# Optimization experiments

Hardware: AMD Instinct MI355X
Metric: run time of the kernel (lower is better)

The kernel has to match this reference:

```python
import jax, jax.numpy as jnp
import numpy as np

B = 32768
NM = 3      # number of modalities (len(mk))
NE = 8      # number of experts
D_IN = 768
D_P = 128   # per-modality projection dim
D_X = D_P * NM  # 384, concatenated feature dim


def setup_inputs() -> dict:
    key = jax.random.key(0)
    ks = jax.random.split(key, 16)
    s = 0.02
    return {
        "feat_text": jax.random.normal(ks[0], (B, D_IN), jnp.float32),
        "feat_audio": jax.random.normal(ks[1], (B, D_IN), jnp.float32),
        "feat_video": jax.random.normal(ks[2], (B, D_IN), jnp.float32),
        "proj_w": jax.random.normal(ks[3], (NM, D_IN, D_P), jnp.float32) * s,
        "proj_b": jax.random.normal(ks[4], (NM, D_P), jnp.float32) * s,
        "exp_w1": jax.random.normal(ks[5], (NE, D_X, D_P), jnp.float32) * s,
        "exp_b1": jax.random.normal(ks[6], (NE, D_P), jnp.float32) * s,
        "exp_w2": jax.random.normal(ks[7], (NE, D_P, D_P), jnp.float32) * s,
        "exp_b2": jax.random.normal(ks[8], (NE, D_P), jnp.float32) * s,
        "gate_w": jax.random.normal(ks[9], (D_X, NE), jnp.float32) * s,
        "gate_b": jax.random.normal(ks[10], (NE,), jnp.float32) * s,
        "pre_w": jax.random.normal(ks[11], (D_P, 64), jnp.float32) * s,
        "pre_b": jax.random.normal(ks[12], (64,), jnp.float32) * s,
        "head_w": jax.random.normal(ks[13], (64, 2), jnp.float32) * s,
        "head_b": jax.random.normal(ks[14], (2,), jnp.float32) * s,
    }


def reference(feat_text, feat_audio, feat_video, proj_w, proj_b,
              exp_w1, exp_b1, exp_w2, exp_b2, gate_w, gate_b,
              pre_w, pre_b, head_w, head_b):
    feats = jnp.stack([feat_text, feat_audio, feat_video], axis=0)  # [M,B,768]
    # per-modality projections, then concat: [B, 128*M]
    proj = jnp.einsum('mbd,mdp->mbp', feats, proj_w) + proj_b[:, None, :]
    x = jnp.concatenate(jnp.split(proj, NM, axis=0), axis=-1)[0]  # [B, 384]
    # gate: softmax over 8 experts
    gw = jax.nn.softmax(x @ gate_w + gate_b, axis=-1)  # [B, 8]
    # all experts as batched GEMM: [E,B,128]
    h = jax.nn.relu(jnp.einsum('bx,exh->ebh', x, exp_w1) + exp_b1[:, None, :])
    eo = jnp.einsum('ebh,eho->ebo', h, exp_w2) + exp_b2[:, None, :]
    fused = jnp.einsum('be,ebh->bh', gw, eo)  # weighted sum over experts
    penult = jax.nn.relu(fused @ pre_w + pre_b)  # Dropout is identity in eval
    logits = penult @ head_w + head_b  # [B, 2]
    return logits
```

## Files before the change

kernel.cpp:

```cpp
#include <hip/hip_runtime.h>
#include <hip/hip_bf16.h>

#define B_ROWS 32768

typedef unsigned short u16;
typedef unsigned int u32;
typedef float f32x4 __attribute__((ext_vector_type(4)));
typedef __bf16 bf16x8 __attribute__((ext_vector_type(8)));

__device__ __forceinline__ u16 f2bf(float f){
    union { float f; u32 u; } v; v.f = f;
    return (u16)((v.u + 0x7FFFu + ((v.u >> 16) & 1u)) >> 16);
}
__device__ __forceinline__ float bf2f(u16 h){
    union { u32 u; float f; } v; v.u = ((u32)h) << 16; return v.f;
}
__device__ __forceinline__ u32 cvtpk(float lo, float hi){
    u32 r;
    asm("v_cvt_pk_bf16_f32 %0, %1, %2" : "=v"(r) : "v"(lo), "v"(hi));
    return r;
}
__device__ __forceinline__ void async_cp16(void* lds_dst, const void* g_src){
    __builtin_amdgcn_global_load_lds(
        (const __attribute__((address_space(1))) unsigned int*)g_src,
        (__attribute__((address_space(3))) unsigned int*)lds_dst, 16, 0, 0);
}

__global__ void cast_weights_kernel(const float* __restrict__ proj_w,
                                    const float* __restrict__ exp_w1,
                                    const float* __restrict__ exp_w2,
                                    const float* __restrict__ pre_w,
                                    const float* __restrict__ gate_w,
                                    u16* __restrict__ pimg, u16* __restrict__ w1img,
                                    u16* __restrict__ w2img, u16* __restrict__ prwT,
                                    u16* __restrict__ gwimg){
    int i = blockIdx.x * 256 + threadIdx.x;
    if (i < 294912){
        int m = i / 98304, r = i % 98304;
        int c = r / 4096, rr = r % 4096;
        int col = rr >> 5, kk = rr & 31;
        int kb = kk ^ (((col >> 1) & 3) << 3);
        pimg[i] = f2bf(proj_w[m*98304 + (c*32 + kb)*128 + col]);
    } else if (i < 688128){
        int j = i - 294912;
        int e = j / 49152, r = j % 49152;
        int ph = r / 4096, rr = r % 4096;
        int q = rr >> 10, col = (rr >> 3) & 127, el = rr & 7;
        w1img[j] = f2bf(exp_w1[e*49152 + (ph*32 + q*8 + el)*128 + col]);
    } else if (i < 819200){
        int j = i - 688128;
        int e = j / 16384, r = j % 16384;
        int c2 = r / 4096, rr = r % 4096;
        int q = rr >> 10, col = (rr >> 3) & 127, el = rr & 7;
        w2img[j] = f2bf(exp_w2[e*16384 + (c2*32 + q*8 + el)*128 + col]);
    } else if (i < 827392){
        int j = i - 819200;
        int o = j / 128, k = j % 128;
        prwT[j] = f2bf(pre_w[k*64 + o]);
    } else if (i < 833536){
        int j = i - 827392;
        int e = j / 384, k = j % 384;
        gwimg[j] = (e < 8) ? f2bf(gate_w[k*8 + e]) : (u16)0;
    }
}

#define XS_OFF   0
#define A_OFF    98304
#define B_OFF    147456
#define HS_OFF   98304
#define GWT_OFF  131072
#define B1_OFF   135168
#define B2_OFF   137216
#define WB_OFF   139264

__global__ __launch_bounds__(512, 1) void fused_kernel(
    const float* __restrict__ ft, const float* __restrict__ fa, const float* __restrict__ fv,
    const u16* __restrict__ pimg, const float* __restrict__ proj_b,
    const u16* __restrict__ w1img, const u16* __restrict__ w2img,
    const u16* __restrict__ prwT, const u16* __restrict__ gwimg,
    const float* __restrict__ gate_b, const float* __restrict__ exp_b1, const float* __restrict__ exp_b2,
    const float* __restrict__ pre_b, const float* __restrict__ head_w, const float* __restrict__ head_b,
    float* __restrict__ out)
{
    __shared__ __align__(16) char lds[163840];
    const int tid = threadIdx.x;
    const int lane = tid & 63, wid = tid >> 6;
    const int wr = wid >> 1, wc = wid & 1;
    const int lr = lane & 15, q = lane >> 4;
    const int blk = blockIdx.x;
    const int row0 = blk * 128;
    const char* w1b = (const char*)w1img;
    const char* w2b = (const char*)w2img;
    char* HsB = lds + HS_OFF;
    u16* b1L = (u16*)(lds + B1_OFF);
    u16* b2L = (u16*)(lds + B2_OFF);

    float pb0[4], pb1[4], pb2[4];
    #pragma unroll
    for (int ni = 0; ni < 4; ni++){
        int c = wc*64 + ni*16 + lr;
        pb0[ni] = proj_b[c];
        pb1[ni] = proj_b[128 + c];
        pb2[ni] = proj_b[256 + c];
    }
    asm volatile("s_waitcnt vmcnt(0)" ::: "memory");

    u32 aoffs[2];
    #pragma unroll
    for (int i = 0; i < 2; i++){
        int P = i*8192 + tid*16;
        int row = P >> 7, inner = P & 127;
        aoffs[i] = (u32)((row0 + row)*3072 + (inner ^ ((row & 7) << 4)));
    }

#define ASTAGE(c) do{                                                          \
        int mm_ = (c) / 24, kk_ = (c) % 24;                                    \
        const char* ab_ = (const char*)(mm_ == 0 ? ft : mm_ == 1 ? fa : fv);   \
        char* la_ = lds + A_OFF + ((c) % 3)*16384 + tid*16;                    \
        async_cp16(la_,        ab_ + aoffs[0] + kk_*128);                      \
        async_cp16(la_ + 8192, ab_ + aoffs[1] + kk_*128);                      \
    }while(0)

#define BSTAGE(c) do{                                                          \
        int mm_ = (c) / 24, kk_ = (c) % 24;                                    \
        async_cp16(lds + B_OFF + ((c) % 2)*8192 + tid*16,                      \
                   (const char*)pimg + mm_*196608 + kk_*8192 + tid*16);        \
    }while(0)

#define PCONSUME(c) do{                                                        \
        const char* Abuf = lds + A_OFF + ((c) % 3)*16384;                      \
        const char* Bbuf = lds + B_OFF + ((c) % 2)*8192;                       \
        bf16x8 af[2];                                                          \
        _Pragma("unroll")                                                      \
        for (int mi = 0; mi < 2; mi++){                                        \
            int row = wr*32 + mi*16 + lr;                                      \
            int aoff = row*128 + ((q*32) ^ ((row & 7) << 4));                  \
            f32x4 a0 = *(const f32x4*)(Abuf + aoff);                           \
            f32x4 a1 = *(const f32x4*)(Abuf + (aoff ^ 16));                    \
            union { u32 w[4]; bf16x8 v; } u;                                   \
            u.w[0] = cvtpk(a0.x, a0.y); u.w[1] = cvtpk(a0.z, a0.w);            \
            u.w[2] = cvtpk(a1.x, a1.y); u.w[3] = cvtpk(a1.z, a1.w);            \
            af[mi] = u.v;                                                      \
        }                                                                      \
        __builtin_amdgcn_s_setprio(1);                                         \
        _Pragma("unroll")                                                      \
        for (int ni = 0; ni < 4; ni++){                                        \
            int col = wc*64 + ni*16 + lr;                                      \
            int boff = col*64 + ((q*16) ^ (((col >> 1) & 3) << 4));            \
            bf16x8 bf = *(const bf16x8*)(Bbuf + boff);                         \
            acc[0][ni] = __builtin_amdgcn_mfma_f32_16x16x32_bf16(af[0], bf, acc[0][ni], 0, 0, 0); \
            acc[1][ni] = __builtin_amdgcn_mfma_f32_16x16x32_bf16(af[1], bf, acc[1][ni], 0, 0, 0); \
        }                                                                      \
        __builtin_amdgcn_s_setprio(0);                                         \
    }while(0)

#define PHASE_A_MOD(MC, PB) do{                                                \
        _Pragma("unroll 1")                                                    \
        for (int kt = 0; kt < 24; kt++){                                       \
            int t = MC*24 + kt;                                                \
            __builtin_amdgcn_sched_barrier(0);                                 \
            __builtin_amdgcn_s_barrier();                                      \
            if (t < 71) BSTAGE(t + 1);                                         \
            if (t < 70) ASTAGE(t + 2);                                         \
            if (t < 70)       asm volatile("s_waitcnt vmcnt(5)" ::: "memory"); \
            else if (t == 70) asm volatile("s_waitcnt vmcnt(3)" ::: "memory"); \
            else              asm volatile("s_waitcnt vmcnt(0)" ::: "memory"); \
            __builtin_amdgcn_s_barrier();                                      \
            __builtin_amdgcn_sched_barrier(0);                                 \
            PCONSUME(t);                                                       \
        }                                                                      \
        _Pragma("unroll")                                                      \
        for (int mi = 0; mi < 2; mi++)                                         \
            _Pragma("unroll")                                                  \
            for (int ni = 0; ni < 4; ni++){                                    \
                int lcol = wc*64 + ni*16 + lr;                                 \
                int colg = MC*128 + lcol;                                      \
                int ktI = colg >> 5, qI = (colg >> 3) & 3, el = colg & 7;      \
                _Pragma("unroll")                                              \
                for (int j = 0; j < 4; j++){                                   \
                    int row = wr*32 + mi*16 + q*4 + j;                         \
                    *(u16*)(lds + (row >> 6)*49152 + ktI*4096 + qI*1024        \
                            + (row & 63)*16 + el*2) = f2bf(acc[mi][ni][j] + PB[ni]); \
                    acc[mi][ni][j] = 0.f;                                      \
                }                                                              \
            }                                                                  \
    }while(0)

    f32x4 acc[2][4];
    #pragma unroll
    for (int i = 0; i < 2; i++)
        #pragma unroll
        for (int j = 0; j < 4; j++) acc[i][j] = {0.f, 0.f, 0.f, 0.f};

    BSTAGE(0); ASTAGE(0); ASTAGE(1);
    PHASE_A_MOD(0, pb0);
    PHASE_A_MOD(1, pb1);
    PHASE_A_MOD(2, pb2);
#undef ASTAGE
#undef BSTAGE
#undef PCONSUME
#undef PHASE_A_MOD

    asm volatile("s_waitcnt lgkmcnt(0)" ::: "memory");
    __builtin_amdgcn_sched_barrier(0);
    __builtin_amdgcn_s_barrier();

    bf16x8 xreg[12][2];
    {
        const char* xa0 = lds + (wr >> 1)*49152 + q*1024;
        #pragma unroll
        for (int ph = 0; ph < 12; ph++){
            xreg[ph][0] = *(const bf16x8*)(xa0 + ph*4096 + ((wr & 1)*32 + lr)*16);
            xreg[ph][1] = *(const bf16x8*)(xa0 + ph*4096 + ((wr & 1)*32 + 16 + lr)*16);
        }
    }

    {
        const char* src = w1b + tid*16;
        async_cp16(lds + WB_OFF + 0*8192 + tid*16, src);
        async_cp16(lds + WB_OFF + 1*8192 + tid*16, src + 8192);
        async_cp16(lds + WB_OFF + 2*8192 + tid*16, src + 16384);
    }
    for (int i = tid; i < 1024; i += 512){
        b1L[i] = f2bf(exp_b1[i]);
        b2L[i] = f2bf(exp_b2[i]);
    }
    {
        f32x4 ga = {0.f, 0.f, 0.f, 0.f};
        const char* xb = lds + (wid >> 2)*49152 + ((wid & 3)*16 + lr)*16 + q*1024;
        const u16* gwp = gwimg + lr*384 + q*8;
        #pragma unroll
        for (int kt = 0; kt < 12; kt++){
            bf16x8 af = *(const bf16x8*)(xb + kt*4096);
            bf16x8 gb = *(const bf16x8*)(gwp + kt*32);
            ga = __builtin_amdgcn_mfma_f32_16x16x32_bf16(af, gb, ga, 0, 0, 0);
        }
        float gbv = gate_b[lr & 7];
        float gw4[4];
        #pragma unroll
        for (int j = 0; j < 4; j++){
            float v = ga[j] + gbv;
            float mx = v;
            mx = fmaxf(mx, __shfl_xor(mx, 1));
            mx = fmaxf(mx, __shfl_xor(mx, 2));
            mx = fmaxf(mx, __shfl_xor(mx, 4));
            float s = __expf(v - mx);
            float t = s;
            t += __shfl_xor(t, 1);
            t += __shfl_xor(t, 2);
            t += __shfl_xor(t, 4);
            gw4[j] = s / t;
        }
        if (lr < 8){
            f32x4 wv = {gw4[0], gw4[1], gw4[2], gw4[3]};
            *(f32x4*)(lds + GWT_OFF + lr*512 + (wid*16 + q*4)*4) = wv;
        }
    }
    asm volatile("s_waitcnt vmcnt(0) lgkmcnt(0)" ::: "memory");
    __builtin_amdgcn_sched_barrier(0);
    __builtin_amdgcn_s_barrier();

#define WGROUP_STAGE(gg2) do{                                                  \
        int e2_ = (gg2) / 6, i2_ = (gg2) % 6;                                  \
        if (i2_ < 4){                                                          \
            const char* src_ = w1b + e2_*98304 + i2_*3*8192 + tid*16;          \
            async_cp16(lds + WB_OFF + 0*8192 + tid*16, src_);                  \
            async_cp16(lds + WB_OFF + 1*8192 + tid*16, src_ + 8192);           \
            async_cp16(lds + WB_OFF + 2*8192 + tid*16, src_ + 16384);          \
        } else {                                                               \
            const char* src_ = w2b + e2_*32768 + (i2_ - 4)*2*8192 + tid*16;    \
            async_cp16(lds + WB_OFF + 0*8192 + tid*16, src_);                  \
            async_cp16(lds + WB_OFF + 1*8192 + tid*16, src_ + 8192);           \
        }                                                                      \
    }while(0)

    f32x4 fus[2][4];
    #pragma unroll
    for (int i = 0; i < 2; i++)
        #pragma unroll
        for (int j = 0; j < 4; j++) fus[i][j] = {0.f, 0.f, 0.f, 0.f};

    #pragma unroll 1
    for (int e = 0; e < 8; e++){
        f32x4 ac1[2][4];
        #pragma unroll
        for (int i = 0; i < 2; i++)
            #pragma unroll
            for (int j = 0; j < 4; j++) ac1[i][j] = {0.f, 0.f, 0.f, 0.f};

        #pragma unroll
        for (int grp = 0; grp < 4; grp++){
            __builtin_amdgcn_s_setprio(1);
            #pragma unroll
            for (int c = 0; c < 3; c++){
                int ph = grp*3 + c;
                const char* wsl = lds + WB_OFF + c*8192 + q*2048;
                #pragma unroll
                for (int ni = 0; ni < 4; ni++){
                    bf16x8 bf = *(const bf16x8*)(wsl + (wc*64 + ni*16 + lr)*16);
                    ac1[0][ni] = __builtin_amdgcn_mfma_f32_16x16x32_bf16(xreg[ph][0], bf, ac1[0][ni], 0, 0, 0);
                    ac1[1][ni] = __builtin_amdgcn_mfma_f32_16x16x32_bf16(xreg[ph][1], bf, ac1[1][ni], 0, 0, 0);
                }
            }
            __builtin_amdgcn_s_setprio(0);
            if (grp == 3){
                #pragma unroll
                for (int mi = 0; mi < 2; mi++)
                    #pragma unroll
                    for (int ni = 0; ni < 4; ni++){
                        int col = wc*64 + ni*16 + lr;
                        float b1v = bf2f(b1L[e*128 + col]);
                        #pragma unroll
                        for (int j = 0; j < 4; j++){
                            int row = wr*32 + mi*16 + q*4 + j;
                            *(u16*)(HsB + row*256 + ((col*2) ^ ((row & 7) << 4)))
                                = f2bf(fmaxf(ac1[mi][ni][j] + b1v, 0.f));
                        }
                    }
                asm volatile("s_waitcnt lgkmcnt(0)" ::: "memory");
            }
            __builtin_amdgcn_sched_barrier(0);
            __builtin_amdgcn_s_barrier();
            WGROUP_STAGE(e*6 + grp + 1);
            asm volatile("s_waitcnt vmcnt(0)" ::: "memory");
            __builtin_amdgcn_s_barrier();
            __builtin_amdgcn_sched_barrier(0);
        }

        f32x4 ac2[2][4];
        #pragma unroll
        for (int i = 0; i < 2; i++)
            #pragma unroll
            for (int j = 0; j < 4; j++) ac2[i][j] = {0.f, 0.f, 0.f, 0.f};

        #pragma unroll 1
        for (int grp = 0; grp < 2; grp++){
            #pragma unroll
            for (int c = 0; c < 2; c++){
                int p2 = grp*2 + c;
                const char* wsl = lds + WB_OFF + c*8192 + q*2048;
                int cb = p2*64 + q*16;
                int rowA = wr*32 + lr;
                int rowB = wr*32 + 16 + lr;
                bf16x8 af0 = *(const bf16x8*)(HsB + rowA*256 + (cb ^ ((rowA & 7) << 4)));
                bf16x8 af1 = *(const bf16x8*)(HsB + rowB*256 + (cb ^ ((rowB & 7) << 4)));
                __builtin_amdgcn_s_setprio(1);
                #pragma unroll
                for (int ni = 0; ni < 4; ni++){
                    bf16x8 bf = *(const bf16x8*)(wsl + (wc*64 + ni*16 + lr)*16);
                    ac2[0][ni] = __builtin_amdgcn_mfma_f32_16x16x32_bf16(af0, bf, ac2[0][ni], 0, 0, 0);
                    ac2[1][ni] = __builtin_amdgcn_mfma_f32_16x16x32_bf16(af1, bf, ac2[1][ni], 0, 0, 0);
                }
                __builtin_amdgcn_s_setprio(0);
            }
            int gg2 = e*6 + 5 + grp;
            __builtin_amdgcn_sched_barrier(0);
            __builtin_amdgcn_s_barrier();
            if (gg2 < 48){
                WGROUP_STAGE(gg2);
                asm volatile("s_waitcnt vmcnt(0)" ::: "memory");
            }
            __builtin_amdgcn_s_barrier();
            __builtin_amdgcn_sched_barrier(0);
        }
        #pragma unroll
        for (int mi = 0; mi < 2; mi++){
            f32x4 gwv = *(const f32x4*)(lds + GWT_OFF + e*512 + (wr*32 + mi*16 + q*4)*4);
            #pragma unroll
            for (int ni = 0; ni < 4; ni++){
                int col = wc*64 + ni*16 + lr;
                float b2v = bf2f(b2L[e*128 + col]);
                #pragma unroll
                for (int j = 0; j < 4; j++)
                    fus[mi][ni][j] += gwv[j] * (ac2[mi][ni][j] + b2v);
            }
        }
    }
#undef WGROUP_STAGE

    __builtin_amdgcn_sched_barrier(0);
    __builtin_amdgcn_s_barrier();
    #pragma unroll
    for (int mi = 0; mi < 2; mi++)
        #pragma unroll
        for (int ni = 0; ni < 4; ni++){
            int col = wc*64 + ni*16 + lr;
            #pragma unroll
            for (int j = 0; j < 4; j++){
                int row = wr*32 + mi*16 + q*4 + j;
                *(u16*)(HsB + row*256 + ((col*2) ^ ((row & 7) << 4))) = f2bf(fus[mi][ni][j]);
            }
        }
    asm volatile("s_waitcnt lgkmcnt(0)" ::: "memory");
    __builtin_amdgcn_sched_barrier(0);
    __builtin_amdgcn_s_barrier();

    f32x4 ap[4];
    #pragma unroll
    for (int i = 0; i < 4; i++) ap[i] = {0.f, 0.f, 0.f, 0.f};
    #pragma unroll
    for (int kt = 0; kt < 4; kt++){
        int row = wid*16 + lr;
        int cb = kt*64 + q*16;
        bf16x8 af = *(const bf16x8*)(HsB + row*256 + (cb ^ ((row & 7) << 4)));
        #pragma unroll
        for (int ni = 0; ni < 4; ni++){
            bf16x8 bf = *(const bf16x8*)(prwT + (size_t)(ni*16 + lr)*128 + kt*32 + q*8);
            ap[ni] = __builtin_amdgcn_mfma_f32_16x16x32_bf16(af, bf, ap[ni], 0, 0, 0);
        }
    }
    float* Pen = (float*)lds;
    #pragma unroll
    for (int ni = 0; ni < 4; ni++){
        int col = ni*16 + lr;
        float pbv = pre_b[col];
        #pragma unroll
        for (int j = 0; j < 4; j++){
            int row = wid*16 + q*4 + j;
            Pen[row*68 + col] = fmaxf(ap[ni][j] + pbv, 0.f);
        }
    }
    asm volatile("s_waitcnt lgkmcnt(0)" ::: "memory");
    __builtin_amdgcn_sched_barrier(0);
    __builtin_amdgcn_s_barrier();
    if (tid < 256){
        int r = tid >> 1, c = tid & 1;
        float s = head_b[c];
        #pragma unroll 8
        for (int k = 0; k < 64; k++) s += Pen[r*68 + k] * head_w[k*2 + c];
        out[(size_t)(blk*128 + r)*2 + c] = s;
    }
}

extern "C" void kernel_launch(void* const* d_in, const int* in_sizes, int n_in,
                              void* d_out, int out_size, void* d_ws, size_t ws_size,
                              hipStream_t stream) {
    const float* ft     = (const float*)d_in[0];
    const float* fa     = (const float*)d_in[1];
    const float* fv     = (const float*)d_in[2];
    const float* proj_w = (const float*)d_in[3];
    const float* proj_b = (const float*)d_in[4];
    const float* exp_w1 = (const float*)d_in[5];
    const float* exp_b1 = (const float*)d_in[6];
    const float* exp_w2 = (const float*)d_in[7];
    const float* exp_b2 = (const float*)d_in[8];
    const float* gate_w = (const float*)d_in[9];
    const float* gate_b = (const float*)d_in[10];
    const float* pre_w  = (const float*)d_in[11];
    const float* pre_b  = (const float*)d_in[12];
    const float* head_w = (const float*)d_in[13];
    const float* head_b = (const float*)d_in[14];
    float* out = (float*)d_out;

    u16* pimg  = (u16*)d_ws;
    u16* w1img = pimg + 294912;
    u16* w2img = w1img + 393216;
    u16* prwT  = w2img + 131072;
    u16* gwimg = prwT + 8192;

    cast_weights_kernel<<<3256, 256, 0, stream>>>(proj_w, exp_w1, exp_w2, pre_w, gate_w,
                                                  pimg, w1img, w2img, prwT, gwimg);
    fused_kernel<<<256, 512, 0, stream>>>(ft, fa, fv, pimg, proj_b,
                                          w1img, w2img, prwT, gwimg,
                                          gate_b, exp_b1, exp_b2,
                                          pre_b, head_w, head_b, out);
}
```

Before: 116.9 us.

## Double-buffer expert weight staging in LDS with two-deep prefetch

Expert weight chunks are now staged into two alternating LDS slots. The next-but-one chunk is prefetched while the current one is consumed, with a partial vmcnt wait in place of a full drain. The LDS layout is moved so H, gate weights, biases and the weight buffers start at offset 0, and the x tile region is reused after it is read into registers. This aims to hide global-to-LDS latency behind MFMA work. In exchange it adds an extra bf16 load for w2 stages so the wait counts stay uniform, and it depends on the x tile being fully consumed before it is overwritten.

```diff
diff --git a/kernel.cpp b/kernel.cpp
--- a/kernel.cpp
+++ b/kernel.cpp
@@ -64,14 +64,13 @@
     }
 }
 
-#define XS_OFF   0
 #define A_OFF    98304
 #define B_OFF    147456
-#define HS_OFF   98304
-#define GWT_OFF  131072
-#define B1_OFF   135168
-#define B2_OFF   137216
-#define WB_OFF   139264
+#define HS2      0
+#define GWT2     32768
+#define B1_2     36864
+#define B2_2     38912
+#define WB2      40960
 
 __global__ __launch_bounds__(512, 1) void fused_kernel(
     const float* __restrict__ ft, const float* __restrict__ fa, const float* __restrict__ fv,
@@ -91,9 +90,9 @@
     const int row0 = blk * 128;
     const char* w1b = (const char*)w1img;
     const char* w2b = (const char*)w2img;
-    char* HsB = lds + HS_OFF;
-    u16* b1L = (u16*)(lds + B1_OFF);
-    u16* b2L = (u16*)(lds + B2_OFF);
+    char* HsB = lds + HS2;
+    u16* b1L = (u16*)(lds + B1_2);
+    u16* b2L = (u16*)(lds + B2_2);
 
     float pb0[4], pb1[4], pb2[4];
     #pragma unroll
@@ -214,17 +213,7 @@
             xreg[ph][1] = *(const bf16x8*)(xa0 + ph*4096 + ((wr & 1)*32 + 16 + lr)*16);
         }
     }
-
-    {
-        const char* src = w1b + tid*16;
-        async_cp16(lds + WB_OFF + 0*8192 + tid*16, src);
-        async_cp16(lds + WB_OFF + 1*8192 + tid*16, src + 8192);
-        async_cp16(lds + WB_OFF + 2*8192 + tid*16, src + 16384);
-    }
-    for (int i = tid; i < 1024; i += 512){
-        b1L[i] = f2bf(exp_b1[i]);
-        b2L[i] = f2bf(exp_b2[i]);
-    }
+    float gw4[4];
     {
         f32x4 ga = {0.f, 0.f, 0.f, 0.f};
         const char* xb = lds + (wid >> 2)*49152 + ((wid & 3)*16 + lr)*16 + q*1024;
@@ -236,7 +225,6 @@
             ga = __builtin_amdgcn_mfma_f32_16x16x32_bf16(af, gb, ga, 0, 0, 0);
         }
         float gbv = gate_b[lr & 7];
-        float gw4[4];
         #pragma unroll
         for (int j = 0; j < 4; j++){
             float v = ga[j] + gbv;
@@ -251,28 +239,40 @@
             t += __shfl_xor(t, 4);
             gw4[j] = s / t;
         }
-        if (lr < 8){
-            f32x4 wv = {gw4[0], gw4[1], gw4[2], gw4[3]};
-            *(f32x4*)(lds + GWT_OFF + lr*512 + (wid*16 + q*4)*4) = wv;
-        }
-    }
-    asm volatile("s_waitcnt vmcnt(0) lgkmcnt(0)" ::: "memory");
-    __builtin_amdgcn_sched_barrier(0);
-    __builtin_amdgcn_s_barrier();
-
-#define WGROUP_STAGE(gg2) do{                                                  \
+    }
+    asm volatile("s_waitcnt lgkmcnt(0)" ::: "memory");
+    __builtin_amdgcn_sched_barrier(0);
+    __builtin_amdgcn_s_barrier();
+
+#define WGROUP_STAGE2(gg2, sl) do{                                             \
         int e2_ = (gg2) / 6, i2_ = (gg2) % 6;                                  \
+        char* dst_ = lds + WB2 + (sl)*24576 + tid*16;                          \
         if (i2_ < 4){                                                          \
-            const char* src_ = w1b + e2_*98304 + i2_*3*8192 + tid*16;          \
-            async_cp16(lds + WB_OFF + 0*8192 + tid*16, src_);                  \
-            async_cp16(lds + WB_OFF + 1*8192 + tid*16, src_ + 8192);           \
-            async_cp16(lds + WB_OFF + 2*8192 + tid*16, src_ + 16384);          \
+            const char* src_ = w1b + e2_*98304 + i2_*24576 + tid*16;           \
+            async_cp16(dst_,         src_);                                    \
+            async_cp16(dst_ + 8192,  src_ + 8192);                             \
+            async_cp16(dst_ + 16384, src_ + 16384);                            \
         } else {                                                               \
-            const char* src_ = w2b + e2_*32768 + (i2_ - 4)*2*8192 + tid*16;    \
-            async_cp16(lds + WB_OFF + 0*8192 + tid*16, src_);                  \
-            async_cp16(lds + WB_OFF + 1*8192 + tid*16, src_ + 8192);           \
+            const char* src_ = w2b + e2_*32768 + (i2_ - 4)*16384 + tid*16;     \
+            async_cp16(dst_,         src_);                                    \
+            async_cp16(dst_ + 8192,  src_ + 8192);                             \
+            async_cp16(dst_ + 16384, src_);            \
         }                                                                      \
     }while(0)
+
+    if (lr < 8){
+        f32x4 wv = {gw4[0], gw4[1], gw4[2], gw4[3]};
+        *(f32x4*)(lds + GWT2 + lr*512 + (wid*16 + q*4)*4) = wv;
+    }
+    for (int i = tid; i < 1024; i += 512){
+        b1L[i] = f2bf(exp_b1[i]);
+        b2L[i] = f2bf(exp_b2[i]);
+    }
+    WGROUP_STAGE2(0, 0);
+    WGROUP_STAGE2(1, 1);
+    asm volatile("s_waitcnt vmcnt(0) lgkmcnt(0)" ::: "memory");
+    __builtin_amdgcn_sched_barrier(0);
+    __builtin_amdgcn_s_barrier();
 
     f32x4 fus[2][4];
     #pragma unroll
@@ -290,11 +290,13 @@
 
         #pragma unroll
         for (int grp = 0; grp < 4; grp++){
+            int g = e*6 + grp;
+            const char* wbase = lds + WB2 + (g & 1)*24576;
             __builtin_amdgcn_s_setprio(1);
             #pragma unroll
             for (int c = 0; c < 3; c++){
                 int ph = grp*3 + c;
-                const char* wsl = lds + WB_OFF + c*8192 + q*2048;
+                const char* wsl = wbase + c*8192 + q*2048;
                 #pragma unroll
                 for (int ni = 0; ni < 4; ni++){
                     bf16x8 bf = *(const bf16x8*)(wsl + (wc*64 + ni*16 + lr)*16);
@@ -321,8 +323,15 @@
             }
             __builtin_amdgcn_sched_barrier(0);
             __builtin_amdgcn_s_barrier();
-            WGROUP_STAGE(e*6 + grp + 1);
-            asm volatile("s_waitcnt vmcnt(0)" ::: "memory");
+            {
+                int gn = g + 2;
+                if (gn < 48){
+                    WGROUP_STAGE2(gn, gn & 1);
+                    asm volatile("s_waitcnt vmcnt(3)" ::: "memory");
+                } else {
+                    asm volatile("s_waitcnt vmcnt(0)" ::: "memory");
+                }
+            }
             __builtin_amdgcn_s_barrier();
             __builtin_amdgcn_sched_barrier(0);
         }
@@ -335,10 +344,12 @@
 
         #pragma unroll 1
         for (int grp = 0; grp < 2; grp++){
+            int g = e*6 + 4 + grp;
+            const char* wbase = lds + WB2 + (g & 1)*24576;
             #pragma unroll
             for (int c = 0; c < 2; c++){
                 int p2 = grp*2 + c;
-                const char* wsl = lds + WB_OFF + c*8192 + q*2048;
+                const char* wsl = wbase + c*8192 + q*2048;
                 int cb = p2*64 + q*16;
                 int rowA = wr*32 + lr;
                 int rowB = wr*32 + 16 + lr;
@@ -353,19 +364,23 @@
                 }
                 __builtin_amdgcn_s_setprio(0);
             }
-            int gg2 = e*6 + 5 + grp;
             __builtin_amdgcn_sched_barrier(0);
             __builtin_amdgcn_s_barrier();
-            if (gg2 < 48){
-                WGROUP_STAGE(gg2);
-                asm volatile("s_waitcnt vmcnt(0)" ::: "memory");
+            {
+                int gn = g + 2;
+                if (gn < 48){
+                    WGROUP_STAGE2(gn, gn & 1);
+                    asm volatile("s_waitcnt vmcnt(3)" ::: "memory");
+                } else {
+                    asm volatile("s_waitcnt vmcnt(0)" ::: "memory");
+                }
             }
             __builtin_amdgcn_s_barrier();
             __builtin_amdgcn_sched_barrier(0);
         }
         #pragma unroll
         for (int mi = 0; mi < 2; mi++){
-            f32x4 gwv = *(const f32x4*)(lds + GWT_OFF + e*512 + (wr*32 + mi*16 + q*4)*4);
+            f32x4 gwv = *(const f32x4*)(lds + GWT2 + e*512 + (wr*32 + mi*16 + q*4)*4);
             #pragma unroll
             for (int ni = 0; ni < 4; ni++){
                 int col = wc*64 + ni*16 + lr;
@@ -376,7 +391,7 @@
             }
         }
     }
-#undef WGROUP_STAGE
+#undef WGROUP_STAGE2
 
     __builtin_amdgcn_sched_barrier(0);
     __builtin_amdgcn_s_barrier();
@@ -409,7 +424,7 @@
             ap[ni] = __builtin_amdgcn_mfma_f32_16x16x32_bf16(af, bf, ap[ni], 0, 0, 0);
         }
     }
-    float* Pen = (float*)lds;
+    float* Pen = (float*)(lds + WB2);
     #pragma unroll
     for (int ni = 0; ni < 4; ni++){
         int col = ni*16 + lr;
```

Result: faster. 104.2 us (-10.9%).
